# Kernel tuning notes

Measured on AMD Instinct MI355X. Metric: run time of the kernel, lower is better.

The kernel has to match this reference:

```python
import jax, jax.numpy as jnp
import numpy as np


def setup_inputs() -> dict:
    key = jax.random.key(0)
    ks = jax.random.split(key, 5)
    B, Lq, Lk, KD, E, VD = 2, 1024, 1024, 128, 128, 128
    return {
        "query": jax.random.normal(ks[0], (B, Lq, KD), dtype=jnp.float32),
        "key": jax.random.normal(ks[1], (B, Lk, KD), dtype=jnp.float32),
        "value": jax.random.normal(ks[2], (B, Lk, VD), dtype=jnp.float32),
        "vT": jax.random.normal(ks[3], (E,), dtype=jnp.float32) * (1.0 / np.sqrt(E)),
        "weight": jax.random.normal(ks[4], (E, 2 * KD), dtype=jnp.float32) * (1.0 / np.sqrt(2 * KD)),
    }


def reference(query, key, value, vT, weight):
    # Additive (Bahdanau) attention: score(i,j) = vT . tanh(W @ concat(q_i, k_j))
    kdim = query.shape[-1]
    Wq = weight[:, :kdim]   # [E, kdim] acts on query half of concat
    Wk = weight[:, kdim:]   # [E, kdim] acts on key half
    qp = jnp.einsum("bqd,ed->bqe", query, Wq)   # [B, Lq, E]
    kp = jnp.einsum("bkd,ed->bke", key, Wk)     # [B, Lk, E]
    # broadcast-add replaces the explicit concat+linear: [B, Lq, Lk, E]
    h = jnp.tanh(qp[:, :, None, :] + kp[:, None, :, :])
    scores = jnp.einsum("bqke,e->bqk", h, vT)    # [B, Lq, Lk]
    attn = jax.nn.softmax(scores, axis=-1)
    return jnp.einsum("bqk,bkv->bqv", attn, value)  # [B, Lq, Vd]
```

## Files before the change

### kernel.cpp

```cpp
#include <hip/hip_runtime.h>

#define CSC 2.88539008177792681f

typedef float v2f __attribute__((ext_vector_type(2)));

__device__ __forceinline__ float fast_exp2(float x) {
  return __builtin_amdgcn_exp2f(x);
}
__device__ __forceinline__ float fast_rcp(float x) {
  return __builtin_amdgcn_rcpf(x);
}
__device__ __forceinline__ v2f vfma(v2f a, v2f b, v2f c) {
  return __builtin_elementwise_fma(a, b, c);
}
__device__ __forceinline__ v2f vsplat(float s) {
  v2f r;
  r[0] = s;
  r[1] = s;
  return r;
}

__global__ __launch_bounds__(256) void proj_kernel(
    const float* __restrict__ query, const float* __restrict__ key,
    const float* __restrict__ weight, float* __restrict__ Eq,
    float* __restrict__ EkT4) {
  __shared__ __align__(16) float rows[16][128];
  __shared__ __align__(16) float tile[16][132];
  int blk = blockIdx.x;
  bool isK = blk >= 128;
  const float* src = isK ? key : query;
  int woff = isK ? 128 : 0;
  int row0 = (isK ? blk - 128 : blk) * 16;
  int tid = threadIdx.x;
#pragma unroll
  for (int i = 0; i < 8; ++i) {
    int f = i * 256 + tid;
    rows[f >> 7][f & 127] = src[(size_t)row0 * 128 + f];
  }
  __syncthreads();
  int e = tid & 127;
  int rh = (tid >> 7) * 8;
  float acc[8];
#pragma unroll
  for (int i = 0; i < 8; ++i) acc[i] = 0.f;
  const float4* wrow =
      reinterpret_cast<const float4*>(weight + (size_t)e * 256 + woff);
#pragma unroll 4
  for (int d4 = 0; d4 < 32; ++d4) {
    float4 wv = wrow[d4];
#pragma unroll
    for (int i = 0; i < 8; ++i) {
      float4 rv = *reinterpret_cast<const float4*>(&rows[rh + i][d4 * 4]);
      acc[i] = fmaf(rv.x, wv.x, acc[i]);
      acc[i] = fmaf(rv.y, wv.y, acc[i]);
      acc[i] = fmaf(rv.z, wv.z, acc[i]);
      acc[i] = fmaf(rv.w, wv.w, acc[i]);
    }
  }
  if (!isK) {
#pragma unroll
    for (int i = 0; i < 8; ++i)
      Eq[(size_t)(row0 + rh + i) * 128 + e] = fast_exp2(CSC * acc[i]);
  } else {
#pragma unroll
    for (int i = 0; i < 8; ++i) tile[rh + i][e] = fast_exp2(CSC * acc[i]);
    __syncthreads();
    int kk = tid & 15;
    int e4a = tid >> 4;
#pragma unroll
    for (int h = 0; h < 2; ++h) {
      int ee = e4a + h * 16;
      float4 v = *reinterpret_cast<const float4*>(&tile[kk][ee * 4]);
      *reinterpret_cast<float4*>(EkT4 + ((size_t)ee * 2048 + row0 + kk) * 4) =
          v;
    }
  }
}

__global__ __launch_bounds__(1024, 4) void attn_kernel(
    const float* __restrict__ Eq, const float* __restrict__ EkT4,
    const float* __restrict__ vT, const float* __restrict__ value,
    float* __restrict__ out) {
  __shared__ __align__(16) float sc[8][1024];
  __shared__ __align__(16) float pout[16][8][128];
  __shared__ float wsum[16][8];
  __shared__ float denom[8];

  int tid = threadIdx.x;
  int lane = tid & 63;
  int w = tid >> 6;
  int b = blockIdx.x >> 7;
  int q0 = (blockIdx.x & 127) * 8;

  {
    const float4* ekp =
        reinterpret_cast<const float4*>(EkT4) + (size_t)b * 1024 + tid;
    const float* eqb = Eq + (size_t)(b * 1024 + q0) * 128;
    const float4* vtp = reinterpret_cast<const float4*>(vT);
    float acc[8];
#pragma unroll
    for (int q = 0; q < 8; ++q) acc[q] = 0.f;
    for (int e4 = 0; e4 < 32; ++e4) {
      float4 ek = ekp[(size_t)e4 * 2048];
      float4 vt4 = vtp[e4];
#pragma unroll
      for (int q = 0; q < 8; ++q) {
        float4 eqq = *reinterpret_cast<const float4*>(
            eqb + (size_t)q * 128 + e4 * 4);
        float A0 = fmaf(eqq.x, ek.x, 1.f);
        float A1 = fmaf(eqq.y, ek.y, 1.f);
        float A2 = fmaf(eqq.z, ek.z, 1.f);
        float A3 = fmaf(eqq.w, ek.w, 1.f);
        float P01 = A0 * A1;
        float P23 = A2 * A3;
        float t01 = fmaf(vt4.x, A1, vt4.y * A0);
        float t23 = fmaf(vt4.z, A3, vt4.w * A2);
        float num = fmaf(t23, P01, t01 * P23);
        acc[q] = fmaf(num, fast_rcp(P01 * P23), acc[q]);
      }
    }
#pragma unroll
    for (int q = 0; q < 8; ++q) {
      float p = fast_exp2(-CSC * acc[q]);
      sc[q][tid] = p;
      float s = p;
#pragma unroll
      for (int off = 32; off; off >>= 1) s += __shfl_xor(s, off);
      if (lane == 0) wsum[w][q] = s;
    }
  }
  __syncthreads();
  if (tid < 8) {
    float s = 0.f;
#pragma unroll
    for (int ww = 0; ww < 16; ++ww) s += wsum[ww][tid];
    denom[tid] = s;
  }

  {
    int kb = w * 64;
    v2f acc2[8];
#pragma unroll
    for (int q = 0; q < 8; ++q) acc2[q] = vsplat(0.f);
    const v2f* vp = reinterpret_cast<const v2f*>(value) +
                    ((size_t)b * 1024 + kb) * 64 + lane;
#pragma unroll 2
    for (int k4 = 0; k4 < 16; ++k4) {
      v2f vv0 = vp[(size_t)(k4 * 4 + 0) * 64];
      v2f vv1 = vp[(size_t)(k4 * 4 + 1) * 64];
      v2f vv2 = vp[(size_t)(k4 * 4 + 2) * 64];
      v2f vv3 = vp[(size_t)(k4 * 4 + 3) * 64];
#pragma unroll
      for (int q = 0; q < 8; ++q) {
        float4 pp = *reinterpret_cast<const float4*>(&sc[q][kb + k4 * 4]);
        acc2[q] = vfma(vsplat(pp.x), vv0, acc2[q]);
        acc2[q] = vfma(vsplat(pp.y), vv1, acc2[q]);
        acc2[q] = vfma(vsplat(pp.z), vv2, acc2[q]);
        acc2[q] = vfma(vsplat(pp.w), vv3, acc2[q]);
      }
    }
#pragma unroll
    for (int q = 0; q < 8; ++q)
      *reinterpret_cast<v2f*>(&pout[w][q][2 * lane]) = acc2[q];
  }
  __syncthreads();

  {
    int q = tid >> 7;
    int c = tid & 127;
    float r = 0.f;
#pragma unroll
    for (int ww = 0; ww < 16; ++ww) r += pout[ww][q][c];
    r *= fast_rcp(denom[q]);
    out[((size_t)b * 1024 + q0 + q) * 128 + c] = r;
  }
}

extern "C" void kernel_launch(void* const* d_in, const int* in_sizes, int n_in,
                              void* d_out, int out_size, void* d_ws,
                              size_t ws_size, hipStream_t stream) {
  const float* query = (const float*)d_in[0];
  const float* key = (const float*)d_in[1];
  const float* value = (const float*)d_in[2];
  const float* vT = (const float*)d_in[3];
  const float* weight = (const float*)d_in[4];
  float* out = (float*)d_out;
  float* Eq = (float*)d_ws;
  float* EkT4 = Eq + 262144;
  proj_kernel<<<256, 256, 0, stream>>>(query, key, weight, Eq, EkT4);
  attn_kernel<<<256, 1024, 0, stream>>>(Eq, EkT4, vT, value, out);
}
```

Baseline: 50.28 us.

## Split attention over key halves with a separate combine kernel

Each attention block now handles 8 queries over half of the keys (512 threads), so the grid doubles from 256 to 512 blocks and spreads better across the GPU's compute units. Partial numerators and softmax denominators go to workspace, and a new combine kernel adds the two halves and normalizes. This works without a running max because the scores are bounded by the tanh form. The cost is an extra kernel launch plus the workspace writes and reads for the partial results.

```diff
diff --git a/kernel.cpp b/kernel.cpp
--- a/kernel.cpp
+++ b/kernel.cpp
@@ -77,29 +77,33 @@
   }
 }
 
-__global__ __launch_bounds__(1024, 4) void attn_kernel(
+__global__ __launch_bounds__(512, 4) void attn_kernel(
     const float* __restrict__ Eq, const float* __restrict__ EkT4,
     const float* __restrict__ vT, const float* __restrict__ value,
-    float* __restrict__ out) {
-  __shared__ __align__(16) float sc[8][1024];
-  __shared__ __align__(16) float pout[16][8][128];
-  __shared__ float wsum[16][8];
-  __shared__ float denom[8];
+    float* __restrict__ pblk, float* __restrict__ dsum) {
+  __shared__ __align__(16) float sc[8][512];
+  __shared__ __align__(16) v2f pout[8][8][64];
+  __shared__ float wsum[8][8];
 
   int tid = threadIdx.x;
   int lane = tid & 63;
   int w = tid >> 6;
-  int b = blockIdx.x >> 7;
-  int q0 = (blockIdx.x & 127) * 8;
+  int bi = blockIdx.x;
+  int kh = bi & 1;
+  int qg = (bi >> 1) & 127;
+  int b = bi >> 8;
+  int q0 = qg * 8;
+  int k0 = kh * 512;
 
   {
-    const float4* ekp =
-        reinterpret_cast<const float4*>(EkT4) + (size_t)b * 1024 + tid;
+    const float4* ekp = reinterpret_cast<const float4*>(EkT4) +
+                        (size_t)b * 1024 + k0 + tid;
     const float* eqb = Eq + (size_t)(b * 1024 + q0) * 128;
     const float4* vtp = reinterpret_cast<const float4*>(vT);
     float acc[8];
 #pragma unroll
     for (int q = 0; q < 8; ++q) acc[q] = 0.f;
+#pragma unroll 2
     for (int e4 = 0; e4 < 32; ++e4) {
       float4 ek = ekp[(size_t)e4 * 2048];
       float4 vt4 = vtp[e4];
@@ -133,8 +137,8 @@
   if (tid < 8) {
     float s = 0.f;
 #pragma unroll
-    for (int ww = 0; ww < 16; ++ww) s += wsum[ww][tid];
-    denom[tid] = s;
+    for (int ww = 0; ww < 8; ++ww) s += wsum[ww][tid];
+    dsum[(size_t)bi * 8 + tid] = s;
   }
 
   {
@@ -143,7 +147,7 @@
 #pragma unroll
     for (int q = 0; q < 8; ++q) acc2[q] = vsplat(0.f);
     const v2f* vp = reinterpret_cast<const v2f*>(value) +
-                    ((size_t)b * 1024 + kb) * 64 + lane;
+                    ((size_t)b * 1024 + k0 + kb) * 64 + lane;
 #pragma unroll 2
     for (int k4 = 0; k4 < 16; ++k4) {
       v2f vv0 = vp[(size_t)(k4 * 4 + 0) * 64];
@@ -160,20 +164,40 @@
       }
     }
 #pragma unroll
-    for (int q = 0; q < 8; ++q)
-      *reinterpret_cast<v2f*>(&pout[w][q][2 * lane]) = acc2[q];
+    for (int q = 0; q < 8; ++q) pout[w][q][lane] = acc2[q];
   }
   __syncthreads();
 
   {
-    int q = tid >> 7;
-    int c = tid & 127;
-    float r = 0.f;
-#pragma unroll
-    for (int ww = 0; ww < 16; ++ww) r += pout[ww][q][c];
-    r *= fast_rcp(denom[q]);
-    out[((size_t)b * 1024 + q0 + q) * 128 + c] = r;
-  }
+    int q = tid >> 6;
+    int c = tid & 63;
+    v2f r = pout[0][q][c];
+#pragma unroll
+    for (int ww = 1; ww < 8; ++ww) r = r + pout[ww][q][c];
+    *reinterpret_cast<v2f*>(pblk + (size_t)bi * 1024 + q * 128 + 2 * c) = r;
+  }
+}
+
+__global__ __launch_bounds__(512) void combine_kernel(
+    const float* __restrict__ pblk, const float* __restrict__ dsum,
+    float* __restrict__ out) {
+  int g = blockIdx.x * 512 + threadIdx.x;
+  int row = g >> 6;
+  int c = g & 63;
+  int b = row >> 10;
+  int qg = (row >> 3) & 127;
+  int q = row & 7;
+  int bi0 = b * 256 + qg * 2;
+  v2f r0 = *reinterpret_cast<const v2f*>(pblk + (size_t)bi0 * 1024 + q * 128 +
+                                         2 * c);
+  v2f r1 = *reinterpret_cast<const v2f*>(pblk + (size_t)(bi0 + 1) * 1024 +
+                                         q * 128 + 2 * c);
+  float d = dsum[(size_t)bi0 * 8 + q] + dsum[(size_t)(bi0 + 1) * 8 + q];
+  v2f r = r0 + r1;
+  float inv = fast_rcp(d);
+  r[0] *= inv;
+  r[1] *= inv;
+  *reinterpret_cast<v2f*>(out + (size_t)row * 128 + 2 * c) = r;
 }
 
 extern "C" void kernel_launch(void* const* d_in, const int* in_sizes, int n_in,
@@ -187,6 +211,9 @@
   float* out = (float*)d_out;
   float* Eq = (float*)d_ws;
   float* EkT4 = Eq + 262144;
+  float* pblk = EkT4 + 262144;
+  float* dsum = pblk + 524288;
   proj_kernel<<<256, 256, 0, stream>>>(query, key, weight, Eq, EkT4);
-  attn_kernel<<<256, 1024, 0, stream>>>(Eq, EkT4, vT, value, out);
-}
+  attn_kernel<<<512, 512, 0, stream>>>(Eq, EkT4, vT, value, pblk, dsum);
+  combine_kernel<<<256, 512, 0, stream>>>(pblk, dsum, out);
+}
```

New measurement: 48.55 us. 3.4% less time.

## Split attention into per-wave key-slice partials with global combine kernel

Applied to the files above, without the earlier changes.

Each wave now handles 4 queries against one 64-key slice and broadcasts probabilities with readlane instead of shared memory. Per-slice outputs and denominators go to global workspace, and a new combine kernel reduces them. The score math is also changed to pair two terms per reciprocal instead of four. This removes shared memory and block barriers and raises block count, at the cost of 16MB of partial-output traffic, an extra kernel launch, and more reciprocal instructions.

```diff
diff --git a/kernel.cpp b/kernel.cpp
--- a/kernel.cpp
+++ b/kernel.cpp
@@ -18,6 +18,9 @@
   r[0] = s;
   r[1] = s;
   return r;
+}
+__device__ __forceinline__ float rdlane(float v, int l) {
+  return __int_as_float(__builtin_amdgcn_readlane(__float_as_int(v), l));
 }
 
 __global__ __launch_bounds__(256) void proj_kernel(
@@ -77,103 +80,102 @@
   }
 }
 
-__global__ __launch_bounds__(1024, 4) void attn_kernel(
+__global__ __launch_bounds__(256, 8) void attn_kernel(
     const float* __restrict__ Eq, const float* __restrict__ EkT4,
     const float* __restrict__ vT, const float* __restrict__ value,
-    float* __restrict__ out) {
-  __shared__ __align__(16) float sc[8][1024];
-  __shared__ __align__(16) float pout[16][8][128];
-  __shared__ float wsum[16][8];
-  __shared__ float denom[8];
-
+    float* __restrict__ pblk, float* __restrict__ dsum) {
   int tid = threadIdx.x;
   int lane = tid & 63;
-  int w = tid >> 6;
-  int b = blockIdx.x >> 7;
-  int q0 = (blockIdx.x & 127) * 8;
+  int gwid = blockIdx.x * 4 + (tid >> 6);
+  int qg = gwid >> 4;
+  int ks = gwid & 15;
+  int b = qg >> 8;
+  int q0 = (qg & 255) * 4;
+  int k0 = ks * 64;
 
+  float p[4];
   {
     const float4* ekp =
-        reinterpret_cast<const float4*>(EkT4) + (size_t)b * 1024 + tid;
-    const float* eqb = Eq + (size_t)(b * 1024 + q0) * 128;
+        reinterpret_cast<const float4*>(EkT4) + (size_t)b * 1024 + k0 + lane;
+    const float* eqb = Eq + ((size_t)b * 1024 + q0) * 128;
     const float4* vtp = reinterpret_cast<const float4*>(vT);
-    float acc[8];
-#pragma unroll
-    for (int q = 0; q < 8; ++q) acc[q] = 0.f;
+    float acc[4] = {0.f, 0.f, 0.f, 0.f};
+#pragma unroll 2
     for (int e4 = 0; e4 < 32; ++e4) {
       float4 ek = ekp[(size_t)e4 * 2048];
       float4 vt4 = vtp[e4];
 #pragma unroll
-      for (int q = 0; q < 8; ++q) {
+      for (int q = 0; q < 4; ++q) {
         float4 eqq = *reinterpret_cast<const float4*>(
             eqb + (size_t)q * 128 + e4 * 4);
         float A0 = fmaf(eqq.x, ek.x, 1.f);
         float A1 = fmaf(eqq.y, ek.y, 1.f);
+        float n0 = fmaf(vt4.x, A1, vt4.y * A0);
+        acc[q] = fmaf(n0, fast_rcp(A0 * A1), acc[q]);
         float A2 = fmaf(eqq.z, ek.z, 1.f);
         float A3 = fmaf(eqq.w, ek.w, 1.f);
-        float P01 = A0 * A1;
-        float P23 = A2 * A3;
-        float t01 = fmaf(vt4.x, A1, vt4.y * A0);
-        float t23 = fmaf(vt4.z, A3, vt4.w * A2);
-        float num = fmaf(t23, P01, t01 * P23);
-        acc[q] = fmaf(num, fast_rcp(P01 * P23), acc[q]);
+        float n1 = fmaf(vt4.z, A3, vt4.w * A2);
+        acc[q] = fmaf(n1, fast_rcp(A2 * A3), acc[q]);
       }
     }
 #pragma unroll
-    for (int q = 0; q < 8; ++q) {
-      float p = fast_exp2(-CSC * acc[q]);
-      sc[q][tid] = p;
-      float s = p;
+    for (int q = 0; q < 4; ++q) {
+      p[q] = fast_exp2(-CSC * acc[q]);
+      float s = p[q];
 #pragma unroll
       for (int off = 32; off; off >>= 1) s += __shfl_xor(s, off);
-      if (lane == 0) wsum[w][q] = s;
+      if (lane == 0) dsum[(size_t)gwid * 4 + q] = s;
     }
-  }
-  __syncthreads();
-  if (tid < 8) {
-    float s = 0.f;
-#pragma unroll
-    for (int ww = 0; ww < 16; ++ww) s += wsum[ww][tid];
-    denom[tid] = s;
   }
 
   {
-    int kb = w * 64;
-    v2f acc2[8];
+    v2f acc2[4];
 #pragma unroll
-    for (int q = 0; q < 8; ++q) acc2[q] = vsplat(0.f);
+    for (int q = 0; q < 4; ++q) acc2[q] = vsplat(0.f);
     const v2f* vp = reinterpret_cast<const v2f*>(value) +
-                    ((size_t)b * 1024 + kb) * 64 + lane;
+                    ((size_t)b * 1024 + k0) * 64 + lane;
 #pragma unroll 2
-    for (int k4 = 0; k4 < 16; ++k4) {
-      v2f vv0 = vp[(size_t)(k4 * 4 + 0) * 64];
-      v2f vv1 = vp[(size_t)(k4 * 4 + 1) * 64];
-      v2f vv2 = vp[(size_t)(k4 * 4 + 2) * 64];
-      v2f vv3 = vp[(size_t)(k4 * 4 + 3) * 64];
+    for (int kg = 0; kg < 16; ++kg) {
+      v2f vv0 = vp[(size_t)(kg * 4 + 0) * 64];
+      v2f vv1 = vp[(size_t)(kg * 4 + 1) * 64];
+      v2f vv2 = vp[(size_t)(kg * 4 + 2) * 64];
+      v2f vv3 = vp[(size_t)(kg * 4 + 3) * 64];
 #pragma unroll
-      for (int q = 0; q < 8; ++q) {
-        float4 pp = *reinterpret_cast<const float4*>(&sc[q][kb + k4 * 4]);
-        acc2[q] = vfma(vsplat(pp.x), vv0, acc2[q]);
-        acc2[q] = vfma(vsplat(pp.y), vv1, acc2[q]);
-        acc2[q] = vfma(vsplat(pp.z), vv2, acc2[q]);
-        acc2[q] = vfma(vsplat(pp.w), vv3, acc2[q]);
+      for (int q = 0; q < 4; ++q) {
+        acc2[q] = vfma(vsplat(rdlane(p[q], kg * 4 + 0)), vv0, acc2[q]);
+        acc2[q] = vfma(vsplat(rdlane(p[q], kg * 4 + 1)), vv1, acc2[q]);
+        acc2[q] = vfma(vsplat(rdlane(p[q], kg * 4 + 2)), vv2, acc2[q]);
+        acc2[q] = vfma(vsplat(rdlane(p[q], kg * 4 + 3)), vv3, acc2[q]);
       }
     }
 #pragma unroll
-    for (int q = 0; q < 8; ++q)
-      *reinterpret_cast<v2f*>(&pout[w][q][2 * lane]) = acc2[q];
+    for (int q = 0; q < 4; ++q)
+      *reinterpret_cast<v2f*>(pblk + (size_t)gwid * 512 + q * 128 + 2 * lane) =
+          acc2[q];
   }
-  __syncthreads();
+}
 
-  {
-    int q = tid >> 7;
-    int c = tid & 127;
-    float r = 0.f;
+__global__ __launch_bounds__(256) void combine_kernel(
+    const float* __restrict__ pblk, const float* __restrict__ dsum,
+    float* __restrict__ out) {
+  int g = blockIdx.x * 256 + threadIdx.x;
+  int row = g >> 6;
+  int c = g & 63;
+  int qg = row >> 2;
+  int q = row & 3;
+  int g0 = qg * 16;
+  v2f r = vsplat(0.f);
+  float d = 0.f;
 #pragma unroll
-    for (int ww = 0; ww < 16; ++ww) r += pout[ww][q][c];
-    r *= fast_rcp(denom[q]);
-    out[((size_t)b * 1024 + q0 + q) * 128 + c] = r;
+  for (int ks = 0; ks < 16; ++ks) {
+    r = r + *reinterpret_cast<const v2f*>(pblk + (size_t)(g0 + ks) * 512 +
+                                          q * 128 + 2 * c);
+    d += dsum[(size_t)(g0 + ks) * 4 + q];
   }
+  float inv = fast_rcp(d);
+  r[0] *= inv;
+  r[1] *= inv;
+  *reinterpret_cast<v2f*>(out + (size_t)row * 128 + 2 * c) = r;
 }
 
 extern "C" void kernel_launch(void* const* d_in, const int* in_sizes, int n_in,
@@ -187,6 +189,9 @@
   float* out = (float*)d_out;
   float* Eq = (float*)d_ws;
   float* EkT4 = Eq + 262144;
+  float* pblk = EkT4 + 262144;
+  float* dsum = pblk + 4194304;
   proj_kernel<<<256, 256, 0, stream>>>(query, key, weight, Eq, EkT4);
-  attn_kernel<<<256, 1024, 0, stream>>>(Eq, EkT4, vT, value, out);
+  attn_kernel<<<2048, 256, 0, stream>>>(Eq, EkT4, vT, value, pblk, dsum);
+  combine_kernel<<<512, 256, 0, stream>>>(pblk, dsum, out);
 }
```

After: 74.63 us. +48.4%, slower.

## Split attention over key chunks into single-wave blocks with separate combine kernel

Applied to the files above, without the earlier changes.

The 1024-thread attention block becomes 4096 independent 64-thread blocks, each handling one 64-key chunk for 8 queries. Each block writes its partial P·V result and partial softmax sum to global workspace, and a new combine kernel adds the 16 chunks and normalises. Block ids are swizzled so neighbouring blocks work on different query groups. This removes block-wide barriers and the shared-memory reduction and gives the scheduler finer work units. In exchange it writes and reads about 16 MB of partials and adds a third kernel launch.

```diff
diff --git a/kernel.cpp b/kernel.cpp
--- a/kernel.cpp
+++ b/kernel.cpp
@@ -77,29 +77,31 @@
   }
 }
 
-__global__ __launch_bounds__(1024, 4) void attn_kernel(
+__global__ __launch_bounds__(64, 4) void attn_kernel(
     const float* __restrict__ Eq, const float* __restrict__ EkT4,
     const float* __restrict__ vT, const float* __restrict__ value,
-    float* __restrict__ out) {
-  __shared__ __align__(16) float sc[8][1024];
-  __shared__ __align__(16) float pout[16][8][128];
-  __shared__ float wsum[16][8];
-  __shared__ float denom[8];
-
-  int tid = threadIdx.x;
-  int lane = tid & 63;
-  int w = tid >> 6;
-  int b = blockIdx.x >> 7;
-  int q0 = (blockIdx.x & 127) * 8;
+    float* __restrict__ pblk, float* __restrict__ dsum) {
+  __shared__ __align__(16) float sc[8][64];
+
+  int lane = threadIdx.x;
+  int bid = blockIdx.x;
+  int ks = bid >> 8;
+  int rr = bid & 255;
+  int qg = (rr & 7) * 32 + (rr >> 3);
+  int b = qg >> 7;
+  int q0 = (qg & 127) * 8;
+  int k0 = ks * 64;
+  int bi = qg * 16 + ks;
 
   {
     const float4* ekp =
-        reinterpret_cast<const float4*>(EkT4) + (size_t)b * 1024 + tid;
+        reinterpret_cast<const float4*>(EkT4) + (size_t)b * 1024 + k0 + lane;
     const float* eqb = Eq + (size_t)(b * 1024 + q0) * 128;
     const float4* vtp = reinterpret_cast<const float4*>(vT);
     float acc[8];
 #pragma unroll
     for (int q = 0; q < 8; ++q) acc[q] = 0.f;
+#pragma unroll 2
     for (int e4 = 0; e4 < 32; ++e4) {
       float4 ek = ekp[(size_t)e4 * 2048];
       float4 vt4 = vtp[e4];
@@ -122,28 +124,21 @@
 #pragma unroll
     for (int q = 0; q < 8; ++q) {
       float p = fast_exp2(-CSC * acc[q]);
-      sc[q][tid] = p;
+      sc[q][lane] = p;
       float s = p;
 #pragma unroll
       for (int off = 32; off; off >>= 1) s += __shfl_xor(s, off);
-      if (lane == 0) wsum[w][q] = s;
+      if (lane == 0) dsum[(size_t)bi * 8 + q] = s;
     }
   }
   __syncthreads();
-  if (tid < 8) {
-    float s = 0.f;
-#pragma unroll
-    for (int ww = 0; ww < 16; ++ww) s += wsum[ww][tid];
-    denom[tid] = s;
-  }
 
   {
-    int kb = w * 64;
     v2f acc2[8];
 #pragma unroll
     for (int q = 0; q < 8; ++q) acc2[q] = vsplat(0.f);
     const v2f* vp = reinterpret_cast<const v2f*>(value) +
-                    ((size_t)b * 1024 + kb) * 64 + lane;
+                    ((size_t)b * 1024 + k0) * 64 + lane;
 #pragma unroll 2
     for (int k4 = 0; k4 < 16; ++k4) {
       v2f vv0 = vp[(size_t)(k4 * 4 + 0) * 64];
@@ -152,7 +147,7 @@
       v2f vv3 = vp[(size_t)(k4 * 4 + 3) * 64];
 #pragma unroll
       for (int q = 0; q < 8; ++q) {
-        float4 pp = *reinterpret_cast<const float4*>(&sc[q][kb + k4 * 4]);
+        float4 pp = *reinterpret_cast<const float4*>(&sc[q][k4 * 4]);
         acc2[q] = vfma(vsplat(pp.x), vv0, acc2[q]);
         acc2[q] = vfma(vsplat(pp.y), vv1, acc2[q]);
         acc2[q] = vfma(vsplat(pp.z), vv2, acc2[q]);
@@ -161,19 +156,32 @@
     }
 #pragma unroll
     for (int q = 0; q < 8; ++q)
-      *reinterpret_cast<v2f*>(&pout[w][q][2 * lane]) = acc2[q];
-  }
-  __syncthreads();
-
-  {
-    int q = tid >> 7;
-    int c = tid & 127;
-    float r = 0.f;
-#pragma unroll
-    for (int ww = 0; ww < 16; ++ww) r += pout[ww][q][c];
-    r *= fast_rcp(denom[q]);
-    out[((size_t)b * 1024 + q0 + q) * 128 + c] = r;
-  }
+      *reinterpret_cast<v2f*>(pblk + (size_t)bi * 1024 + q * 128 + 2 * lane) =
+          acc2[q];
+  }
+}
+
+__global__ __launch_bounds__(256) void combine_kernel(
+    const float* __restrict__ pblk, const float* __restrict__ dsum,
+    float* __restrict__ out) {
+  int g = blockIdx.x * 256 + threadIdx.x;
+  int row = g >> 6;
+  int c = g & 63;
+  int qg = row >> 3;
+  int q = row & 7;
+  int g0 = qg * 16;
+  v2f r = vsplat(0.f);
+  float d = 0.f;
+#pragma unroll
+  for (int ks = 0; ks < 16; ++ks) {
+    r = r + *reinterpret_cast<const v2f*>(pblk + (size_t)(g0 + ks) * 1024 +
+                                          q * 128 + 2 * c);
+    d += dsum[(size_t)(g0 + ks) * 8 + q];
+  }
+  float inv = fast_rcp(d);
+  r[0] *= inv;
+  r[1] *= inv;
+  *reinterpret_cast<v2f*>(out + (size_t)row * 128 + 2 * c) = r;
 }
 
 extern "C" void kernel_launch(void* const* d_in, const int* in_sizes, int n_in,
@@ -187,6 +195,9 @@
   float* out = (float*)d_out;
   float* Eq = (float*)d_ws;
   float* EkT4 = Eq + 262144;
+  float* pblk = EkT4 + 262144;
+  float* dsum = pblk + 4194304;
   proj_kernel<<<256, 256, 0, stream>>>(query, key, weight, Eq, EkT4);
-  attn_kernel<<<256, 1024, 0, stream>>>(Eq, EkT4, vT, value, out);
-}
+  attn_kernel<<<4096, 64, 0, stream>>>(Eq, EkT4, vT, value, pblk, dsum);
+  combine_kernel<<<512, 256, 0, stream>>>(pblk, dsum, out);
+}
```

New measurement: 54.81 us. +9.0%, slower.
